# Optimization experiments

Measured on AMD Instinct MI355X. Metric: run time of the kernel, lower is better.

Reference implementation:

```python
import jax, jax.numpy as jnp
import numpy as np

B, S, H = 2, 2048, 2048
NH, NKV = 16, 4
HD = H // NH            # 128
GROUPS = NH // NKV      # 4
ROTARY_BASE = 10000.0
NEG = -1e9


def setup_inputs() -> dict:
    key = jax.random.key(0)
    ks = jax.random.split(key, 6)
    x = jax.random.normal(ks[0], (B, S, H), dtype=jnp.float32)
    # additive causal mask [B,1,S,S]
    causal = jnp.where(jnp.tril(jnp.ones((S, S), dtype=bool)), 0.0, NEG).astype(jnp.float32)
    attention_mask = jnp.broadcast_to(causal[None, None], (B, 1, S, S))
    position_ids = jnp.broadcast_to(jnp.arange(S, dtype=jnp.int32)[None], (B, S))
    sc = 0.02
    Wq = jax.random.normal(ks[1], (H, NH * HD), dtype=jnp.float32) * sc
    Wk = jax.random.normal(ks[2], (H, NKV * HD), dtype=jnp.float32) * sc
    Wv = jax.random.normal(ks[3], (H, NKV * HD), dtype=jnp.float32) * sc
    Wo = jax.random.normal(ks[4], (H, H), dtype=jnp.float32) * sc
    return {"x": x, "attention_mask": attention_mask, "position_ids": position_ids,
            "Wq": Wq, "Wk": Wk, "Wv": Wv, "Wo": Wo}


def _rotate_half(t):
    t1, t2 = t[..., : HD // 2], t[..., HD // 2:]
    return jnp.concatenate((-t2, t1), axis=-1)


def _rope_sin_cos(position_ids, dtype):
    inv_freq = 1.0 / (ROTARY_BASE ** (jnp.arange(0, HD, 2, dtype=jnp.float32) / HD))  # [HD/2]
    freqs = position_ids.astype(jnp.float32)[..., None] * inv_freq[None, None, :]      # [B,S,HD/2]
    emb = jnp.concatenate((freqs, freqs), axis=-1)                                     # [B,S,HD]
    return jnp.sin(emb).astype(dtype), jnp.cos(emb).astype(dtype)


def reference(x, attention_mask, position_ids, Wq, Wk, Wv, Wo):
    # QKV projections (no bias)
    q = (x @ Wq).reshape(B, S, NH, HD).transpose(0, 2, 1, 3)     # [B,NH,S,HD]
    k = (x @ Wk).reshape(B, S, NKV, HD).transpose(0, 2, 1, 3)    # [B,NKV,S,HD]
    v = (x @ Wv).reshape(B, S, NKV, HD).transpose(0, 2, 1, 3)
    sin, cos = _rope_sin_cos(position_ids, x.dtype)
    sin, cos = sin[:, None], cos[:, None]                         # unsqueeze head dim
    q = q * cos + _rotate_half(q) * sin
    k = k * cos + _rotate_half(k) * sin
    # GQA: repeat kv heads
    k = jnp.repeat(k, GROUPS, axis=1)                             # [B,NH,S,HD]
    v = jnp.repeat(v, GROUPS, axis=1)
    scores = jnp.einsum('bhqd,bhkd->bhqk', q, k) / jnp.sqrt(jnp.asarray(HD, x.dtype))
    scores = scores + attention_mask                              # additive causal mask
    attn = jax.nn.softmax(scores.astype(jnp.float32), axis=-1).astype(x.dtype)
    # dropout p=0.0 -> no-op
    out = jnp.einsum('bhqk,bhkd->bhqd', attn, v)                  # [B,NH,S,HD]
    out = out.transpose(0, 2, 1, 3).reshape(B, S, H)
    return out @ Wo
```

## Files before the change

### kernel.cpp

```cpp
#include <hip/hip_runtime.h>
#include <hip/hip_bf16.h>
#include <stdint.h>
#include <math.h>

#define B_ 2
#define S_ 2048
#define H_ 2048
#define NH_ 16
#define NKV_ 4
#define HD_ 128

typedef __bf16 bf16;
typedef __bf16 bf16x8 __attribute__((ext_vector_type(8)));
typedef __bf16 bf16x4 __attribute__((ext_vector_type(4)));
typedef float f32x4 __attribute__((ext_vector_type(4)));

__device__ __forceinline__ void async_copy16(const void* g, void* l) {
  __builtin_amdgcn_global_load_lds(
      (const __attribute__((address_space(1))) void*)(uintptr_t)g,
      (__attribute__((address_space(3))) void*)(uintptr_t)l,
      16, 0, 0);
}

__device__ __forceinline__ f32x4 mfma16(bf16x8 a, bf16x8 b, f32x4 c) {
  return __builtin_amdgcn_mfma_f32_16x16x32_bf16(a, b, c, 0, 0, 0);
}


__global__ void f32_to_bf16_k(const float* __restrict__ in, bf16* __restrict__ o, int n) {
  int i = (blockIdx.x * 256 + threadIdx.x) * 4;
  if (i >= n) return;
  float4 v = *(const float4*)(in + i);
  bf16x4 r;
  r[0] = (bf16)v.x; r[1] = (bf16)v.y; r[2] = (bf16)v.z; r[3] = (bf16)v.w;
  *(bf16x4*)(o + i) = r;
}

__global__ void transpose_all_k(const float* __restrict__ Wq, const float* __restrict__ Wk,
                                const float* __restrict__ Wv, const float* __restrict__ Wo,
                                bf16* __restrict__ WqkvT, bf16* __restrict__ WoT) {
  __shared__ float tile[32][33];
  int bid = blockIdx.x;
  const float* W; bf16* Wt; int N, bx, by;
  if (bid < 4096)      { W = Wq; Wt = WqkvT;                          N = 2048; int b2 = bid;        bx = b2 & 63; by = b2 >> 6; }
  else if (bid < 5120) { W = Wk; Wt = WqkvT + (size_t)2048 * 2048;    N = 512;  int b2 = bid - 4096; bx = b2 & 15; by = b2 >> 4; }
  else if (bid < 6144) { W = Wv; Wt = WqkvT + (size_t)2560 * 2048;    N = 512;  int b2 = bid - 5120; bx = b2 & 15; by = b2 >> 4; }
  else                 { W = Wo; Wt = WoT;                            N = 2048; int b2 = bid - 6144; bx = b2 & 63; by = b2 >> 6; }
  const int K = 2048;
  int n0 = bx * 32, k0 = by * 32;
  int tx = threadIdx.x, ty = threadIdx.y;
#pragma unroll
  for (int j = 0; j < 32; j += 8)
    tile[ty + j][tx] = W[(size_t)(k0 + ty + j) * N + n0 + tx];
  __syncthreads();
#pragma unroll
  for (int j = 0; j < 32; j += 8)
    Wt[(size_t)(n0 + ty + j) * K + k0 + tx] = (bf16)tile[tx][ty + j];
}

__global__ void rope_table_k(float2* __restrict__ tab) {
  int i = blockIdx.x * 256 + threadIdx.x;
  int p = i >> 6, d = i & 63;
  float invf = expf(-((float)(2 * d) / 128.0f) * 9.210340371976184f);
  float fr = (float)p * invf;
  float sv, cv;
  sincosf(fr, &sv, &cv);
  tab[i] = make_float2(cv, sv);
}

__global__ void rope_apply_v8_k(bf16* __restrict__ t, const int* __restrict__ pos_ids,
                                const float2* __restrict__ tab, int hshift, int hmask,
                                float scale) {
  int i = blockIdx.x * 256 + threadIdx.x;
  int g = i & 7;
  int tmp = i >> 3;
  int h = tmp & hmask;
  int row = tmp >> hshift;
  int pos = pos_ids[row];
  size_t base = (((size_t)row << hshift) + h) * HD_ + g * 8;
  const float2* tb = tab + pos * 64 + g * 8;
  bf16x8 lo = *(const bf16x8*)(t + base);
  bf16x8 hi = *(const bf16x8*)(t + base + 64);
  float4 t0 = *(const float4*)(tb);
  float4 t1 = *(const float4*)(tb + 2);
  float4 t2 = *(const float4*)(tb + 4);
  float4 t3 = *(const float4*)(tb + 6);
  float cs[8], sn[8];
  cs[0]=t0.x; sn[0]=t0.y; cs[1]=t0.z; sn[1]=t0.w;
  cs[2]=t1.x; sn[2]=t1.y; cs[3]=t1.z; sn[3]=t1.w;
  cs[4]=t2.x; sn[4]=t2.y; cs[5]=t2.z; sn[5]=t2.w;
  cs[6]=t3.x; sn[6]=t3.y; cs[7]=t3.z; sn[7]=t3.w;
  bf16x8 olo, ohi;
#pragma unroll
  for (int j = 0; j < 8; ++j) {
    float a = (float)lo[j], b = (float)hi[j];
    olo[j] = (bf16)((a * cs[j] - b * sn[j]) * scale);
    ohi[j] = (bf16)((b * cs[j] + a * sn[j]) * scale);
  }
  *(bf16x8*)(t + base) = olo;
  *(bf16x8*)(t + base + 64) = ohi;
}


template <int MODE, int NJ>
__global__ __launch_bounds__(512) void gemm256_k(const bf16* __restrict__ A,
                                                 const bf16* __restrict__ Bt,
                                                 void* __restrict__ C0,
                                                 void* __restrict__ C1,
                                                 void* __restrict__ C2,
                                                 int M, int N, int K) {
  extern __shared__ __align__(16) char smem[];
  constexpr int BUFSZ = 32768 + NJ * 8192;
  const int tid = threadIdx.x;
  const int lane = tid & 63;
  const int w = tid >> 6;
  const int wm = w >> 2;
  const int wn = w & 3;
  const int g16 = lane >> 4, c16 = lane & 15;
  const int row0 = blockIdx.y * 256;
  const int col0 = blockIdx.x * (NJ * 64);
  const int srow = tid >> 3;
  const int sslot = tid & 7;
  const int ldsw = w * 1024;

  auto stage = [&](int buf, int kt, int r) {
    int rr = (r < 4) ? r : r - 4;
    int row = rr * 64 + srow;
    int ss = sslot ^ (row & 7);
    const bf16* src = (r < 4) ? (A + (size_t)(row0 + row) * K)
                              : (Bt + (size_t)(col0 + row) * K);
    async_copy16(src + (kt << 6) + ss * 8,
                 smem + buf * BUFSZ + ((r < 4) ? 0 : 32768) + rr * 8192 + ldsw);
  };

  int offA[2][8], offB[2][NJ];
#pragma unroll
  for (int ks = 0; ks < 2; ++ks) {
#pragma unroll
    for (int i = 0; i < 8; ++i) {
      int ra = wm * 128 + i * 16 + c16;
      offA[ks][i] = ra * 128 + (((ks * 4 + g16) ^ (ra & 7)) << 4);
    }
#pragma unroll
    for (int j = 0; j < NJ; ++j) {
      int rb = wn * (16 * NJ) + j * 16 + c16;
      offB[ks][j] = 32768 + rb * 128 + (((ks * 4 + g16) ^ (rb & 7)) << 4);
    }
  }

  const f32x4 fz = {0.f, 0.f, 0.f, 0.f};
  f32x4 acc[8][NJ];
#pragma unroll
  for (int i = 0; i < 8; ++i)
#pragma unroll
    for (int j = 0; j < NJ; ++j) acc[i][j] = fz;

  const int nkt = K >> 6;
#pragma unroll
  for (int r = 0; r < 4 + NJ; ++r) stage(0, 0, r);
  asm volatile("s_waitcnt vmcnt(0)" ::: "memory");
  __builtin_amdgcn_s_barrier();

  for (int t = 0; t < nkt; ++t) {
    const char* Ab = smem + (t & 1) * BUFSZ;
    const bool pf = (t + 1 < nkt);
    const int nb = (t + 1) & 1;
    bf16x8 bfr[2][NJ];

    {
      bf16x8 af[2][2];
#pragma unroll
      for (int ks = 0; ks < 2; ++ks) {
#pragma unroll
        for (int j = 0; j < NJ; ++j) bfr[ks][j] = *(const bf16x8*)(Ab + offB[ks][j]);
        af[ks][0] = *(const bf16x8*)(Ab + offA[ks][0]);
        af[ks][1] = *(const bf16x8*)(Ab + offA[ks][1]);
      }
      if (pf) { stage(nb, t + 1, 0); stage(nb, t + 1, 1); stage(nb, t + 1, 2); stage(nb, t + 1, 3); }
      __builtin_amdgcn_s_barrier();
      asm volatile("s_waitcnt lgkmcnt(0)" ::: "memory");
      __builtin_amdgcn_sched_barrier(0);
      __builtin_amdgcn_s_setprio(1);
#pragma unroll
      for (int ks = 0; ks < 2; ++ks)
#pragma unroll
        for (int m = 0; m < 2; ++m)
#pragma unroll
          for (int j = 0; j < NJ; ++j)
            acc[m][j] = mfma16(af[ks][m], bfr[ks][j], acc[m][j]);
      __builtin_amdgcn_s_setprio(0);
      __builtin_amdgcn_sched_barrier(0);
      __builtin_amdgcn_s_barrier();
    }

#pragma unroll
    for (int q = 1; q < 4; ++q) {
      bf16x8 af[2][2];
#pragma unroll
      for (int ks = 0; ks < 2; ++ks) {
        af[ks][0] = *(const bf16x8*)(Ab + offA[ks][q * 2]);
        af[ks][1] = *(const bf16x8*)(Ab + offA[ks][q * 2 + 1]);
      }
      if (q == 1 && pf) {
#pragma unroll
        for (int r = 0; r < NJ; ++r) stage(nb, t + 1, 4 + r);
      }
      __builtin_amdgcn_s_barrier();
      asm volatile("s_waitcnt lgkmcnt(0)" ::: "memory");
      __builtin_amdgcn_sched_barrier(0);
      __builtin_amdgcn_s_setprio(1);
#pragma unroll
      for (int ks = 0; ks < 2; ++ks)
#pragma unroll
        for (int m = 0; m < 2; ++m)
#pragma unroll
          for (int j = 0; j < NJ; ++j)
            acc[q * 2 + m][j] = mfma16(af[ks][m], bfr[ks][j], acc[q * 2 + m][j]);
      __builtin_amdgcn_s_setprio(0);
      __builtin_amdgcn_sched_barrier(0);
      if (q == 3 && pf) asm volatile("s_waitcnt vmcnt(0)" ::: "memory");
      __builtin_amdgcn_s_barrier();
    }
  }

#pragma unroll
  for (int i = 0; i < 8; ++i) {
    int gr0 = row0 + wm * 128 + i * 16 + g16 * 4;
#pragma unroll
    for (int j = 0; j < NJ; ++j) {
      int gc = col0 + wn * (16 * NJ) + j * 16 + c16;
      if constexpr (MODE == 2) {
        if (gc < 2048) {
#pragma unroll
          for (int r = 0; r < 4; ++r)
            ((bf16*)C0)[(size_t)(gr0 + r) * 2048 + gc] = (bf16)acc[i][j][r];
        } else if (gc < 2560) {
#pragma unroll
          for (int r = 0; r < 4; ++r)
            ((bf16*)C1)[(size_t)(gr0 + r) * 512 + (gc - 2048)] = (bf16)acc[i][j][r];
        } else {
          int dv = gc - 2560;
          int hkv = dv >> 7, d = dv & 127;
          size_t va = (((size_t)(gr0 >> 11) * NKV_ + hkv) * HD_ + d) * S_ + (gr0 & 2047);
          bf16x4 pk;
#pragma unroll
          for (int r = 0; r < 4; ++r) pk[r] = (bf16)acc[i][j][r];
          *(bf16x4*)((bf16*)C2 + va) = pk;
        }
      } else {
#pragma unroll
        for (int r = 0; r < 4; ++r) {
          if constexpr (MODE == 1)
            ((float*)C0)[(size_t)(gr0 + r) * N + gc] = acc[i][j][r];
          else
            ((bf16*)C0)[(size_t)(gr0 + r) * N + gc] = (bf16)acc[i][j][r];
        }
      }
    }
  }
}


template <int MODE>
__global__ __launch_bounds__(512) void gemm8_k(const bf16* __restrict__ A,
                                               const bf16* __restrict__ Bt,
                                               void* __restrict__ C0,
                                               void* __restrict__ C1,
                                               void* __restrict__ C2,
                                               int M, int N, int K) {
  extern __shared__ __align__(16) char smem[];
  const int tid = threadIdx.x;
  const int lane = tid & 63;
  const int w = tid >> 6;
  const int wm = w >> 2;
  const int wn = w & 3;
  const int g16 = lane >> 4, c16 = lane & 15;
  const int row0 = blockIdx.y * 128;
  const int col0 = blockIdx.x * 256;
  const int srow = tid >> 3;
  const int sslot = tid & 7;
  const int ldsw = w * 1024;

  auto stageA = [&](int s, int kt, int r) {
    int row = r * 64 + srow;
    int ss = sslot ^ (row & 7);
    async_copy16(A + (size_t)(row0 + row) * K + (kt << 6) + ss * 8,
                 smem + s * 49152 + r * 8192 + ldsw);
  };
  auto stageB = [&](int s, int kt, int r) {
    int row = r * 64 + srow;
    int ss = sslot ^ (row & 7);
    async_copy16(Bt + (size_t)(col0 + row) * K + (kt << 6) + ss * 8,
                 smem + s * 49152 + 16384 + r * 8192 + ldsw);
  };

  int offA[2][4], offB[2][4];
#pragma unroll
  for (int ks = 0; ks < 2; ++ks) {
#pragma unroll
    for (int i = 0; i < 4; ++i) {
      int ra = wm * 64 + i * 16 + c16;
      offA[ks][i] = ra * 128 + (((ks * 4 + g16) ^ (ra & 7)) << 4);
      int rb = wn * 64 + i * 16 + c16;
      offB[ks][i] = rb * 128 + (((ks * 4 + g16) ^ (rb & 7)) << 4);
    }
  }

  const f32x4 fz = {0.f, 0.f, 0.f, 0.f};
  f32x4 acc[4][4];
#pragma unroll
  for (int i = 0; i < 4; ++i)
#pragma unroll
    for (int j = 0; j < 4; ++j) acc[i][j] = fz;

  const int nkt = K >> 6;
#pragma unroll
  for (int r = 0; r < 2; ++r) stageA(0, 0, r);
#pragma unroll
  for (int r = 0; r < 4; ++r) stageB(0, 0, r);
#pragma unroll
  for (int r = 0; r < 2; ++r) stageA(1, 1, r);
#pragma unroll
  for (int r = 0; r < 4; ++r) stageB(1, 1, r);
  asm volatile("s_waitcnt vmcnt(6)" ::: "memory");
  __builtin_amdgcn_s_barrier();

  int ct = 0, pt = 2;
  for (int t = 0; t < nkt; ++t) {
    const char* Ab = smem + ct * 49152;
    const char* Bb = Ab + 16384;
    const bool pf = (t + 2 < nkt);
    const int kpf = t + 2;
    bf16x8 af[4], bfr[4];

#pragma unroll
    for (int i = 0; i < 4; ++i) af[i] = *(const bf16x8*)(Ab + offA[0][i]);
#pragma unroll
    for (int j = 0; j < 4; ++j) bfr[j] = *(const bf16x8*)(Bb + offB[0][j]);
    if (pf) { stageA(pt, kpf, 0); stageA(pt, kpf, 1); stageB(pt, kpf, 0); }
    __builtin_amdgcn_s_barrier();
    asm volatile("s_waitcnt lgkmcnt(0)" ::: "memory");
    __builtin_amdgcn_sched_barrier(0);
    __builtin_amdgcn_s_setprio(1);
#pragma unroll
    for (int i = 0; i < 4; ++i)
#pragma unroll
      for (int j = 0; j < 4; ++j) acc[i][j] = mfma16(af[i], bfr[j], acc[i][j]);
    __builtin_amdgcn_s_setprio(0);
    __builtin_amdgcn_sched_barrier(0);
    __builtin_amdgcn_s_barrier();

#pragma unroll
    for (int i = 0; i < 4; ++i) af[i] = *(const bf16x8*)(Ab + offA[1][i]);
#pragma unroll
    for (int j = 0; j < 4; ++j) bfr[j] = *(const bf16x8*)(Bb + offB[1][j]);
    if (pf) { stageB(pt, kpf, 1); stageB(pt, kpf, 2); stageB(pt, kpf, 3); }
    if (pf) asm volatile("s_waitcnt vmcnt(6)" ::: "memory");
    else    asm volatile("s_waitcnt vmcnt(0)" ::: "memory");
    __builtin_amdgcn_s_barrier();
    asm volatile("s_waitcnt lgkmcnt(0)" ::: "memory");
    __builtin_amdgcn_sched_barrier(0);
    __builtin_amdgcn_s_setprio(1);
#pragma unroll
    for (int i = 0; i < 4; ++i)
#pragma unroll
      for (int j = 0; j < 4; ++j) acc[i][j] = mfma16(af[i], bfr[j], acc[i][j]);
    __builtin_amdgcn_s_setprio(0);
    __builtin_amdgcn_sched_barrier(0);
    __builtin_amdgcn_s_barrier();

    ct = (ct == 2) ? 0 : ct + 1;
    pt = (pt == 2) ? 0 : pt + 1;
  }

#pragma unroll
  for (int i = 0; i < 4; ++i) {
    int gr0 = row0 + wm * 64 + i * 16 + g16 * 4;
#pragma unroll
    for (int j = 0; j < 4; ++j) {
      int gc = col0 + wn * 64 + j * 16 + c16;
#pragma unroll
      for (int r = 0; r < 4; ++r) {
        if constexpr (MODE == 1)
          ((float*)C0)[(size_t)(gr0 + r) * N + gc] = acc[i][j][r];
        else
          ((bf16*)C0)[(size_t)(gr0 + r) * N + gc] = (bf16)acc[i][j][r];
      }
    }
  }
}


__global__ __launch_bounds__(256, 2) void attn_fwd_k(const bf16* __restrict__ Qg,
                                                     const bf16* __restrict__ Kg,
                                                     const bf16* __restrict__ VTg,
                                                     bf16* __restrict__ Og) {
  __shared__ __align__(16) bf16 Ks[2][64 * 128];
  __shared__ __align__(16) bf16 Vt[3][128 * 64];

  const int tid = threadIdx.x;
  const int lane = tid & 63;
  const int w = tid >> 6;
  const int g16 = lane >> 4;
  const int c16 = lane & 15;

  int bid = blockIdx.x;
  int rr_ = bid >> 5, bh = bid & 31;
  int qb = (rr_ < 8) ? (15 - rr_) : (rr_ - 8);
  const int b = bh >> 4;
  const int h = bh & 15;
  const int hkv = h >> 2;
  const int q0 = qb * 128;
  const int qw = q0 + w * 32;

  bf16x8 qf[2][4];
#pragma unroll
  for (int nq = 0; nq < 2; ++nq)
#pragma unroll
    for (int ksq = 0; ksq < 4; ++ksq)
      qf[nq][ksq] = *(const bf16x8*)(Qg + ((size_t)(b * S_ + qw + nq * 16 + c16) * NH_ + h) * HD_ + (ksq * 4 + g16) * 8);

  float m_run[2] = {-1e30f, -1e30f};
  float l_run[2] = {0.f, 0.f};
  const f32x4 fz = {0.f, 0.f, 0.f, 0.f};
  f32x4 acc[2][8];
#pragma unroll
  for (int nq = 0; nq < 2; ++nq)
#pragma unroll
    for (int dt = 0; dt < 8; ++dt) acc[nq][dt] = fz;

  const size_t kbase = ((size_t)b * S_ * NKV_ + hkv) * HD_;
  const size_t vbase = ((size_t)(b * NKV_ + hkv)) * HD_ * S_;

  auto stageK = [&](int buf, int kv0) {
#pragma unroll
    for (int rd = 0; rd < 4; ++rd) {
      int Lb = rd * 256 + w * 64;
      int row = (Lb + lane) >> 4;
      int ssl = (lane & 15) ^ (row & 7);
      async_copy16(Kg + kbase + (size_t)(kv0 + row) * (NKV_ * HD_) + ssl * 8,
                   (char*)&Ks[buf][0] + Lb * 16);
    }
  };
  auto stageV = [&](int buf, int kv0) {
#pragma unroll
    for (int rd = 0; rd < 4; ++rd) {
      int Lb = rd * 256 + w * 64;
      int row = (Lb + lane) >> 3;
      int ssl = (lane & 7) ^ (row & 7);
      async_copy16(VTg + vbase + (size_t)row * S_ + kv0 + ssl * 8,
                   (char*)&Vt[buf][0] + Lb * 16);
    }
  };

  const int ntiles = 2 * qb + 2;
  stageK(0, 0);
  stageV(0, 0);

  bf16x8 pa[2][2];
  bool pend = false;
  int vb_pend = 0;
  int vbt = 0;

  for (int t = 0; t < ntiles; ++t) {
    __syncthreads();
    int vbn = (vbt == 2) ? 0 : vbt + 1;
    if (t + 1 < ntiles) { stageK((t + 1) & 1, (t + 1) * 64); stageV(vbn, (t + 1) * 64); }
    const int kv0 = t * 64;
    const bool g = (kv0 <= qw + 31);

    f32x4 sc[2][4];
    if (g) {
      const char* KsC = (const char*)&Ks[t & 1][0];
#pragma unroll
      for (int nq = 0; nq < 2; ++nq)
#pragma unroll
        for (int mt = 0; mt < 4; ++mt) sc[nq][mt] = fz;

      __builtin_amdgcn_s_setprio(1);
#pragma unroll
      for (int ksq = 0; ksq < 4; ++ksq) {
        bf16x8 kf[4];
#pragma unroll
        for (int mt = 0; mt < 4; ++mt) {
          int gp = c16 >> 2, rp = c16 & 3;
          int blk = 8 * (mt >> 1) + 2 * gp + ((mt & 1) ^ (gp & 1));
          int row = blk * 4 + rp;
          kf[mt] = *(const bf16x8*)(KsC + row * 256 + (((ksq * 4 + g16) ^ (row & 7)) << 4));
        }
#pragma unroll
        for (int nq = 0; nq < 2; ++nq)
#pragma unroll
          for (int mt = 0; mt < 4; ++mt)
            sc[nq][mt] = mfma16(kf[mt], qf[nq][ksq], sc[nq][mt]);
      }
      __builtin_amdgcn_s_setprio(0);
    }

    if (pend) {
      const char* VtP = (const char*)&Vt[vb_pend][0];
      __builtin_amdgcn_s_setprio(1);
#pragma unroll
      for (int ks = 0; ks < 2; ++ks)
#pragma unroll
        for (int dt = 0; dt < 8; ++dt) {
          int rv = dt * 16 + c16;
          bf16x8 vf = *(const bf16x8*)(VtP + rv * 128 + (((ks * 4 + g16) ^ (rv & 7)) << 4));
          acc[0][dt] = mfma16(vf, pa[0][ks], acc[0][dt]);
          acc[1][dt] = mfma16(vf, pa[1][ks], acc[1][dt]);
        }
      __builtin_amdgcn_s_setprio(0);
      pend = false;
    }

    if (g) {
      if (kv0 + 63 > qw) {
#pragma unroll
        for (int nq = 0; nq < 2; ++nq) {
          int qa = qw + nq * 16 + c16;
#pragma unroll
          for (int mt = 0; mt < 4; ++mt) {
            int blk = 8 * (mt >> 1) + 2 * g16 + ((mt & 1) ^ (g16 & 1));
#pragma unroll
            for (int r = 0; r < 4; ++r) {
              int ka = kv0 + blk * 4 + r;
              if (ka > qa) sc[nq][mt][r] = -1e30f;
            }
          }
        }
      }

      float mx[2];
#pragma unroll
      for (int nq = 0; nq < 2; ++nq) {
        float v = sc[nq][0][0];
#pragma unroll
        for (int mt = 0; mt < 4; ++mt)
#pragma unroll
          for (int r = 0; r < 4; ++r) v = fmaxf(v, sc[nq][mt][r]);
        v = fmaxf(v, __shfl_xor(v, 16));
        v = fmaxf(v, __shfl_xor(v, 32));
        mx[nq] = v;
      }
      if (__any((mx[0] > m_run[0] + 8.f) || (mx[1] > m_run[1] + 8.f))) {
#pragma unroll
        for (int nq = 0; nq < 2; ++nq) {
          float mn = fmaxf(m_run[nq], mx[nq]);
          float corr = exp2f(m_run[nq] - mn);
          m_run[nq] = mn;
          l_run[nq] *= corr;
#pragma unroll
          for (int dt = 0; dt < 8; ++dt) acc[nq][dt] *= corr;
        }
      }
#pragma unroll
      for (int nq = 0; nq < 2; ++nq) {
        float sum = 0.f;
#pragma unroll
        for (int mt = 0; mt < 4; ++mt)
#pragma unroll
          for (int r = 0; r < 4; ++r) {
            float p = exp2f(sc[nq][mt][r] - m_run[nq]);
            sc[nq][mt][r] = p;
            sum += p;
          }
        sum += __shfl_xor(sum, 16);
        sum += __shfl_xor(sum, 32);
        l_run[nq] += sum;
      }

#pragma unroll
      for (int nq = 0; nq < 2; ++nq)
#pragma unroll
        for (int ks = 0; ks < 2; ++ks) {
          f32x4 sA = (g16 & 1) ? sc[nq][2 * ks + 1] : sc[nq][2 * ks];
          f32x4 sB = (g16 & 1) ? sc[nq][2 * ks] : sc[nq][2 * ks + 1];
          bf16x8 tf;
          tf[0] = (bf16)sA[0]; tf[1] = (bf16)sA[1]; tf[2] = (bf16)sA[2]; tf[3] = (bf16)sA[3];
          tf[4] = (bf16)sB[0]; tf[5] = (bf16)sB[1]; tf[6] = (bf16)sB[2]; tf[7] = (bf16)sB[3];
          pa[nq][ks] = tf;
        }
      pend = true;
      vb_pend = vbt;
    }
    vbt = vbn;
  }

  if (pend) {
    const char* VtP = (const char*)&Vt[vb_pend][0];
#pragma unroll
    for (int ks = 0; ks < 2; ++ks)
#pragma unroll
      for (int dt = 0; dt < 8; ++dt) {
        int rv = dt * 16 + c16;
        bf16x8 vf = *(const bf16x8*)(VtP + rv * 128 + (((ks * 4 + g16) ^ (rv & 7)) << 4));
        acc[0][dt] = mfma16(vf, pa[0][ks], acc[0][dt]);
        acc[1][dt] = mfma16(vf, pa[1][ks], acc[1][dt]);
      }
  }

#pragma unroll
  for (int nq = 0; nq < 2; ++nq) {
    float inv = 1.0f / l_run[nq];
    size_t base = ((size_t)(b * S_ + qw + nq * 16 + c16) * NH_ + h) * HD_ + g16 * 4;
#pragma unroll
    for (int dt = 0; dt < 8; ++dt) {
      bf16x4 ov;
#pragma unroll
      for (int r = 0; r < 4; ++r) ov[r] = (bf16)(acc[nq][dt][r] * inv);
      *(bf16x4*)(Og + base + dt * 16) = ov;
    }
  }
}


extern "C" void kernel_launch(void* const* d_in, const int* in_sizes, int n_in,
                              void* d_out, int out_size, void* d_ws, size_t ws_size,
                              hipStream_t stream) {
  const float* x  = (const float*)d_in[0];
  const int* pos  = (const int*)d_in[2];
  const float* Wq = (const float*)d_in[3];
  const float* Wk = (const float*)d_in[4];
  const float* Wv = (const float*)d_in[5];
  const float* Wo = (const float*)d_in[6];

  char* ws = (char*)d_ws;
  size_t off = 0;
  auto alloc = [&](size_t bytes) -> char* {
    char* p = ws + off;
    off += (bytes + 255) & ~(size_t)255;
    return p;
  };
  const size_t rows = (size_t)B_ * S_;
  bf16* xb    = (bf16*)alloc(rows * H_ * 2);
  bf16* bq    = (bf16*)alloc(rows * (NH_ * HD_) * 2);
  bf16* batt  = (bf16*)alloc(rows * (NH_ * HD_) * 2);
  bf16* WqkvT = (bf16*)alloc((size_t)3072 * H_ * 2);
  bf16* WoT   = (bf16*)alloc((size_t)H_ * H_ * 2);
  bf16* bk    = (bf16*)alloc(rows * (NKV_ * HD_) * 2);
  bf16* VT    = (bf16*)alloc(rows * (NKV_ * HD_) * 2);
  float2* tab = (float2*)alloc((size_t)S_ * 64 * sizeof(float2));

  auto* fqkv = gemm256_k<2, 3>;
  auto* fo   = gemm8_k<1>;
  const int lds256 = 2 * (32768 + 3 * 8192);
  const int lds8   = 3 * 49152;
  bool big =
      (hipFuncSetAttribute((const void*)fqkv, hipFuncAttributeMaxDynamicSharedMemorySize, lds256) == hipSuccess) &&
      (hipFuncSetAttribute((const void*)fo, hipFuncAttributeMaxDynamicSharedMemorySize, lds8) == hipSuccess);

  f32_to_bf16_k<<<(rows * H_) / (256 * 4), 256, 0, stream>>>(x, xb, rows * H_);
  transpose_all_k<<<10240, dim3(32, 8), 0, stream>>>(Wq, Wk, Wv, Wo, WqkvT, WoT);
  rope_table_k<<<(S_ * 64) / 256, 256, 0, stream>>>(tab);

  gemm256_k<2, 3><<<dim3(16, 16), 512, lds256, stream>>>(xb, WqkvT, bq, bk, VT, 4096, 3072, 2048);
  (void)big;

  rope_apply_v8_k<<<(4096 * NH_ * 8) / 256, 256, 0, stream>>>(bq, pos, tab, 4, 15, 0.12753102f);
  rope_apply_v8_k<<<(4096 * NKV_ * 8) / 256, 256, 0, stream>>>(bk, pos, tab, 2, 3, 1.0f);

  attn_fwd_k<<<dim3(512), 256, 0, stream>>>(bq, bk, VT, batt);

  gemm8_k<1><<<dim3(8, 32), 512, lds8, stream>>>(batt, WoT, d_out, nullptr, nullptr, 4096, 2048, 2048);
}
```

Measured before the change: 199.2 us.

## Pair mirrored query blocks per workgroup for causal balance, drop deferred PV pipeline

Each attention workgroup now processes two 16-row query fragments per wave, one from a late query block and one from the mirrored early block, so every workgroup covers a roughly equal number of KV tiles under the causal mask. The deferred P·V software pipeline with triple-buffered V is removed in favour of a simpler double-buffered K/V stage where P·V runs in the same iteration as QK. This is meant to balance causal work across blocks and reduce LDS use. The cost is that the overlap between the softmax of one tile and the PV MFMAs of the previous tile is lost, and waves whose fragments are masked out sit idle in those tiles.

```diff
diff --git a/kernel.cpp b/kernel.cpp
--- a/kernel.cpp
+++ b/kernel.cpp
@@ -396,7 +396,7 @@
                                                      const bf16* __restrict__ VTg,
                                                      bf16* __restrict__ Og) {
   __shared__ __align__(16) bf16 Ks[2][64 * 128];
-  __shared__ __align__(16) bf16 Vt[3][128 * 64];
+  __shared__ __align__(16) bf16 Vt[2][128 * 64];
 
   const int tid = threadIdx.x;
   const int lane = tid & 63;
@@ -404,21 +404,22 @@
   const int g16 = lane >> 4;
   const int c16 = lane & 15;
 
-  int bid = blockIdx.x;
-  int rr_ = bid >> 5, bh = bid & 31;
-  int qb = (rr_ < 8) ? (15 - rr_) : (rr_ - 8);
+  const int bid = blockIdx.x;
+  const int bh = bid & 31;
+  const int z = (bid >> 5) & 1;
+  const int p = bid >> 6;
   const int b = bh >> 4;
   const int h = bh & 15;
   const int hkv = h >> 2;
-  const int q0 = qb * 128;
-  const int qw = q0 + w * 32;
+  const int qfb0 = (15 - p) * 128 + z * 64 + w * 16;
+  const int qfb1 = p * 128 + z * 64 + w * 16;
 
   bf16x8 qf[2][4];
 #pragma unroll
-  for (int nq = 0; nq < 2; ++nq)
-#pragma unroll
-    for (int ksq = 0; ksq < 4; ++ksq)
-      qf[nq][ksq] = *(const bf16x8*)(Qg + ((size_t)(b * S_ + qw + nq * 16 + c16) * NH_ + h) * HD_ + (ksq * 4 + g16) * 8);
+  for (int ksq = 0; ksq < 4; ++ksq) {
+    qf[0][ksq] = *(const bf16x8*)(Qg + ((size_t)(b * S_ + qfb0 + c16) * NH_ + h) * HD_ + (ksq * 4 + g16) * 8);
+    qf[1][ksq] = *(const bf16x8*)(Qg + ((size_t)(b * S_ + qfb1 + c16) * NH_ + h) * HD_ + (ksq * 4 + g16) * 8);
+  }
 
   float m_run[2] = {-1e30f, -1e30f};
   float l_run[2] = {0.f, 0.f};
@@ -432,7 +433,7 @@
   const size_t kbase = ((size_t)b * S_ * NKV_ + hkv) * HD_;
   const size_t vbase = ((size_t)(b * NKV_ + hkv)) * HD_ * S_;
 
-  auto stageK = [&](int buf, int kv0) {
+  auto stage = [&](int buf, int kv0) {
 #pragma unroll
     for (int rd = 0; rd < 4; ++rd) {
       int Lb = rd * 256 + w * 64;
@@ -441,8 +442,6 @@
       async_copy16(Kg + kbase + (size_t)(kv0 + row) * (NKV_ * HD_) + ssl * 8,
                    (char*)&Ks[buf][0] + Lb * 16);
     }
-  };
-  auto stageV = [&](int buf, int kv0) {
 #pragma unroll
     for (int rd = 0; rd < 4; ++rd) {
       int Lb = rd * 256 + w * 64;
@@ -453,156 +452,119 @@
     }
   };
 
-  const int ntiles = 2 * qb + 2;
-  stageK(0, 0);
-  stageV(0, 0);
-
-  bf16x8 pa[2][2];
-  bool pend = false;
-  int vb_pend = 0;
-  int vbt = 0;
+  const int ntiles = 32 - 2 * p;
+  stage(0, 0);
+  int cur = 0;
 
   for (int t = 0; t < ntiles; ++t) {
     __syncthreads();
-    int vbn = (vbt == 2) ? 0 : vbt + 1;
-    if (t + 1 < ntiles) { stageK((t + 1) & 1, (t + 1) * 64); stageV(vbn, (t + 1) * 64); }
+    if (t + 1 < ntiles) stage(cur ^ 1, (t + 1) * 64);
     const int kv0 = t * 64;
-    const bool g = (kv0 <= qw + 31);
+    const bool good[2] = { kv0 <= qfb0 + 15, kv0 <= qfb1 + 15 };
+
+    const bf16* KsC = &Ks[cur][0];
+    const bf16* VtC = &Vt[cur][0];
 
     f32x4 sc[2][4];
-    if (g) {
-      const char* KsC = (const char*)&Ks[t & 1][0];
-#pragma unroll
-      for (int nq = 0; nq < 2; ++nq)
-#pragma unroll
-        for (int mt = 0; mt < 4; ++mt) sc[nq][mt] = fz;
-
-      __builtin_amdgcn_s_setprio(1);
-#pragma unroll
-      for (int ksq = 0; ksq < 4; ++ksq) {
-        bf16x8 kf[4];
+#pragma unroll
+    for (int nq = 0; nq < 2; ++nq)
+#pragma unroll
+      for (int mt = 0; mt < 4; ++mt) sc[nq][mt] = fz;
+
+    __builtin_amdgcn_s_setprio(1);
+#pragma unroll
+    for (int ksq = 0; ksq < 4; ++ksq) {
+      bf16x8 kf[4];
+#pragma unroll
+      for (int mt = 0; mt < 4; ++mt) {
+        int gp = c16 >> 2, rp = c16 & 3;
+        int blk = 8 * (mt >> 1) + 2 * gp + ((mt & 1) ^ (gp & 1));
+        int row = blk * 4 + rp;
+        kf[mt] = *(const bf16x8*)((const char*)KsC + row * 256 + (((ksq * 4 + g16) ^ (row & 7)) << 4));
+      }
+      if (good[0])
+#pragma unroll
+        for (int mt = 0; mt < 4; ++mt) sc[0][mt] = mfma16(kf[mt], qf[0][ksq], sc[0][mt]);
+      if (good[1])
+#pragma unroll
+        for (int mt = 0; mt < 4; ++mt) sc[1][mt] = mfma16(kf[mt], qf[1][ksq], sc[1][mt]);
+    }
+    __builtin_amdgcn_s_setprio(0);
+
+    bf16x8 pa[2][2];
+#pragma unroll
+    for (int nq = 0; nq < 2; ++nq) {
+      if (!good[nq]) continue;
+      const int qfb = nq ? qfb1 : qfb0;
+      if (kv0 + 63 > qfb) {
+        int qa = qfb + c16;
 #pragma unroll
         for (int mt = 0; mt < 4; ++mt) {
-          int gp = c16 >> 2, rp = c16 & 3;
-          int blk = 8 * (mt >> 1) + 2 * gp + ((mt & 1) ^ (gp & 1));
-          int row = blk * 4 + rp;
-          kf[mt] = *(const bf16x8*)(KsC + row * 256 + (((ksq * 4 + g16) ^ (row & 7)) << 4));
-        }
-#pragma unroll
-        for (int nq = 0; nq < 2; ++nq)
-#pragma unroll
-          for (int mt = 0; mt < 4; ++mt)
-            sc[nq][mt] = mfma16(kf[mt], qf[nq][ksq], sc[nq][mt]);
-      }
-      __builtin_amdgcn_s_setprio(0);
-    }
-
-    if (pend) {
-      const char* VtP = (const char*)&Vt[vb_pend][0];
-      __builtin_amdgcn_s_setprio(1);
-#pragma unroll
-      for (int ks = 0; ks < 2; ++ks)
-#pragma unroll
-        for (int dt = 0; dt < 8; ++dt) {
-          int rv = dt * 16 + c16;
-          bf16x8 vf = *(const bf16x8*)(VtP + rv * 128 + (((ks * 4 + g16) ^ (rv & 7)) << 4));
-          acc[0][dt] = mfma16(vf, pa[0][ks], acc[0][dt]);
-          acc[1][dt] = mfma16(vf, pa[1][ks], acc[1][dt]);
-        }
-      __builtin_amdgcn_s_setprio(0);
-      pend = false;
-    }
-
-    if (g) {
-      if (kv0 + 63 > qw) {
-#pragma unroll
-        for (int nq = 0; nq < 2; ++nq) {
-          int qa = qw + nq * 16 + c16;
-#pragma unroll
-          for (int mt = 0; mt < 4; ++mt) {
-            int blk = 8 * (mt >> 1) + 2 * g16 + ((mt & 1) ^ (g16 & 1));
-#pragma unroll
-            for (int r = 0; r < 4; ++r) {
-              int ka = kv0 + blk * 4 + r;
-              if (ka > qa) sc[nq][mt][r] = -1e30f;
-            }
+          int blk = 8 * (mt >> 1) + 2 * g16 + ((mt & 1) ^ (g16 & 1));
+#pragma unroll
+          for (int r = 0; r < 4; ++r) {
+            int ka = kv0 + blk * 4 + r;
+            if (ka > qa) sc[nq][mt][r] = -1e30f;
           }
         }
       }
-
-      float mx[2];
-#pragma unroll
-      for (int nq = 0; nq < 2; ++nq) {
-        float v = sc[nq][0][0];
-#pragma unroll
-        for (int mt = 0; mt < 4; ++mt)
-#pragma unroll
-          for (int r = 0; r < 4; ++r) v = fmaxf(v, sc[nq][mt][r]);
-        v = fmaxf(v, __shfl_xor(v, 16));
-        v = fmaxf(v, __shfl_xor(v, 32));
-        mx[nq] = v;
-      }
-      if (__any((mx[0] > m_run[0] + 8.f) || (mx[1] > m_run[1] + 8.f))) {
-#pragma unroll
-        for (int nq = 0; nq < 2; ++nq) {
-          float mn = fmaxf(m_run[nq], mx[nq]);
-          float corr = exp2f(m_run[nq] - mn);
-          m_run[nq] = mn;
-          l_run[nq] *= corr;
-#pragma unroll
-          for (int dt = 0; dt < 8; ++dt) acc[nq][dt] *= corr;
+      float v = sc[nq][0][0];
+#pragma unroll
+      for (int mt = 0; mt < 4; ++mt)
+#pragma unroll
+        for (int r = 0; r < 4; ++r) v = fmaxf(v, sc[nq][mt][r]);
+      v = fmaxf(v, __shfl_xor(v, 16));
+      v = fmaxf(v, __shfl_xor(v, 32));
+      if (__any(v > m_run[nq] + 8.f)) {
+        float mn = fmaxf(m_run[nq], v);
+        float corr = exp2f(m_run[nq] - mn);
+        m_run[nq] = mn;
+        l_run[nq] *= corr;
+#pragma unroll
+        for (int dt = 0; dt < 8; ++dt) acc[nq][dt] *= corr;
+      }
+      float sum = 0.f;
+#pragma unroll
+      for (int mt = 0; mt < 4; ++mt)
+#pragma unroll
+        for (int r = 0; r < 4; ++r) {
+          float pv = exp2f(sc[nq][mt][r] - m_run[nq]);
+          sc[nq][mt][r] = pv;
+          sum += pv;
         }
-      }
-#pragma unroll
-      for (int nq = 0; nq < 2; ++nq) {
-        float sum = 0.f;
-#pragma unroll
-        for (int mt = 0; mt < 4; ++mt)
-#pragma unroll
-          for (int r = 0; r < 4; ++r) {
-            float p = exp2f(sc[nq][mt][r] - m_run[nq]);
-            sc[nq][mt][r] = p;
-            sum += p;
-          }
-        sum += __shfl_xor(sum, 16);
-        sum += __shfl_xor(sum, 32);
-        l_run[nq] += sum;
-      }
-
-#pragma unroll
-      for (int nq = 0; nq < 2; ++nq)
-#pragma unroll
-        for (int ks = 0; ks < 2; ++ks) {
-          f32x4 sA = (g16 & 1) ? sc[nq][2 * ks + 1] : sc[nq][2 * ks];
-          f32x4 sB = (g16 & 1) ? sc[nq][2 * ks] : sc[nq][2 * ks + 1];
-          bf16x8 tf;
-          tf[0] = (bf16)sA[0]; tf[1] = (bf16)sA[1]; tf[2] = (bf16)sA[2]; tf[3] = (bf16)sA[3];
-          tf[4] = (bf16)sB[0]; tf[5] = (bf16)sB[1]; tf[6] = (bf16)sB[2]; tf[7] = (bf16)sB[3];
-          pa[nq][ks] = tf;
-        }
-      pend = true;
-      vb_pend = vbt;
-    }
-    vbt = vbn;
-  }
-
-  if (pend) {
-    const char* VtP = (const char*)&Vt[vb_pend][0];
+      sum += __shfl_xor(sum, 16);
+      sum += __shfl_xor(sum, 32);
+      l_run[nq] += sum;
+#pragma unroll
+      for (int ks = 0; ks < 2; ++ks) {
+        f32x4 sA = (g16 & 1) ? sc[nq][2 * ks + 1] : sc[nq][2 * ks];
+        f32x4 sB = (g16 & 1) ? sc[nq][2 * ks] : sc[nq][2 * ks + 1];
+        bf16x8 tf;
+        tf[0] = (bf16)sA[0]; tf[1] = (bf16)sA[1]; tf[2] = (bf16)sA[2]; tf[3] = (bf16)sA[3];
+        tf[4] = (bf16)sB[0]; tf[5] = (bf16)sB[1]; tf[6] = (bf16)sB[2]; tf[7] = (bf16)sB[3];
+        pa[nq][ks] = tf;
+      }
+    }
+
+    __builtin_amdgcn_s_setprio(1);
 #pragma unroll
     for (int ks = 0; ks < 2; ++ks)
 #pragma unroll
       for (int dt = 0; dt < 8; ++dt) {
         int rv = dt * 16 + c16;
-        bf16x8 vf = *(const bf16x8*)(VtP + rv * 128 + (((ks * 4 + g16) ^ (rv & 7)) << 4));
-        acc[0][dt] = mfma16(vf, pa[0][ks], acc[0][dt]);
-        acc[1][dt] = mfma16(vf, pa[1][ks], acc[1][dt]);
-      }
+        bf16x8 vf = *(const bf16x8*)((const char*)VtC + rv * 128 + (((ks * 4 + g16) ^ (rv & 7)) << 4));
+        if (good[0]) acc[0][dt] = mfma16(vf, pa[0][ks], acc[0][dt]);
+        if (good[1]) acc[1][dt] = mfma16(vf, pa[1][ks], acc[1][dt]);
+      }
+    __builtin_amdgcn_s_setprio(0);
+    cur ^= 1;
   }
 
 #pragma unroll
   for (int nq = 0; nq < 2; ++nq) {
+    const int qfb = nq ? qfb1 : qfb0;
     float inv = 1.0f / l_run[nq];
-    size_t base = ((size_t)(b * S_ + qw + nq * 16 + c16) * NH_ + h) * HD_ + g16 * 4;
+    size_t base = ((size_t)(b * S_ + qfb + c16) * NH_ + h) * HD_ + g16 * 4;
 #pragma unroll
     for (int dt = 0; dt < 8; ++dt) {
       bf16x4 ov;
@@ -645,16 +607,14 @@
   auto* fo   = gemm8_k<1>;
   const int lds256 = 2 * (32768 + 3 * 8192);
   const int lds8   = 3 * 49152;
-  bool big =
-      (hipFuncSetAttribute((const void*)fqkv, hipFuncAttributeMaxDynamicSharedMemorySize, lds256) == hipSuccess) &&
-      (hipFuncSetAttribute((const void*)fo, hipFuncAttributeMaxDynamicSharedMemorySize, lds8) == hipSuccess);
+  (void)hipFuncSetAttribute((const void*)fqkv, hipFuncAttributeMaxDynamicSharedMemorySize, lds256);
+  (void)hipFuncSetAttribute((const void*)fo, hipFuncAttributeMaxDynamicSharedMemorySize, lds8);
 
   f32_to_bf16_k<<<(rows * H_) / (256 * 4), 256, 0, stream>>>(x, xb, rows * H_);
   transpose_all_k<<<10240, dim3(32, 8), 0, stream>>>(Wq, Wk, Wv, Wo, WqkvT, WoT);
   rope_table_k<<<(S_ * 64) / 256, 256, 0, stream>>>(tab);
 
   gemm256_k<2, 3><<<dim3(16, 16), 512, lds256, stream>>>(xb, WqkvT, bq, bk, VT, 4096, 3072, 2048);
-  (void)big;
 
   rope_apply_v8_k<<<(4096 * NH_ * 8) / 256, 256, 0, stream>>>(bq, pos, tab, 4, 15, 0.12753102f);
   rope_apply_v8_k<<<(4096 * NKV_ * 8) / 256, 256, 0, stream>>>(bk, pos, tab, 2, 3, 1.0f);
```

Measured after the change: 203.4 us. 1.02x slower.
